# Optimization experiments

Measured on AMD Instinct MI355X. Metric: run time of the kernel, lower is better.

The kernel has to match this reference:

```python
import jax, jax.numpy as jnp
import numpy as np

HIDDEN = 128
OUT_EMB = 256
OUT_CH = 1
NUM_LAYERS = 3
NUM_EDGES = 1000000
NUM_NODES = 50000


def glorot_orthogonal(key, shape, scale=2.0):
    # orthogonal init then rescale variance like DIG's glorot_orthogonal
    W = jax.nn.initializers.orthogonal()(key, shape, jnp.float32)
    W = W * jnp.sqrt(scale / ((shape[0] + shape[1]) * jnp.var(W)))
    return W


def setup_inputs() -> dict:
    key = jax.random.key(0)
    ks = jax.random.split(key, 8)
    e2 = jax.random.normal(ks[0], (NUM_EDGES, HIDDEN), dtype=jnp.float32)
    i = jax.random.randint(ks[1], (NUM_EDGES,), 0, NUM_NODES, dtype=jnp.int64)
    W_up = glorot_orthogonal(ks[2], (OUT_EMB, HIDDEN))
    b_up = jnp.zeros((OUT_EMB,), jnp.float32)
    Ws = jnp.stack([glorot_orthogonal(k, (OUT_EMB, OUT_EMB)) for k in jax.random.split(ks[3], NUM_LAYERS)])
    bs = jnp.zeros((NUM_LAYERS, OUT_EMB), jnp.float32)
    W_out = glorot_orthogonal(ks[4], (OUT_CH, OUT_EMB))
    return {"e2": e2, "i": i, "W_up": W_up, "b_up": b_up,
            "Ws": Ws, "bs": bs, "W_out": W_out, "num_nodes": NUM_NODES}


def reference(e2, i, W_up, b_up, Ws, bs, W_out, num_nodes):
    # scatter-sum edge messages into nodes: v[n] = sum_{k: i[k]==n} e2[k]
    v = jax.ops.segment_sum(e2, i, num_segments=num_nodes)  # [N, HIDDEN]
    v = v @ W_up.T + b_up                                   # [N, OUT_EMB]
    for l in range(NUM_LAYERS):
        v = jax.nn.silu(v @ Ws[l].T + bs[l])
    return v @ W_out.T                                      # [N, OUT_CH]
```

## Files before the change

kernel.cpp:

```cpp
#include <hip/hip_runtime.h>

#define HIDDEN 128
#define OUT_EMB 256
#define NLAYERS 3
#define TM 64
#define LDA 264

typedef __bf16 bf16x8 __attribute__((ext_vector_type(8)));
typedef float f32x4 __attribute__((ext_vector_type(4)));

__device__ __forceinline__ unsigned short f2bf(float x) {
    union { float f; unsigned u; } c; c.f = x;
    unsigned r = c.u + 0x7fff + ((c.u >> 16) & 1);
    return (unsigned short)(r >> 16);
}
__device__ __forceinline__ float bf2f(unsigned short h) {
    union { unsigned u; float f; } c; c.u = ((unsigned)h) << 16;
    return c.f;
}

__global__ __launch_bounds__(256) void hist_kernel(
    const int* __restrict__ idx, int* __restrict__ counts, int ne)
{
    int e = blockIdx.x * 256 + threadIdx.x;
    if (e < ne) atomicAdd(&counts[idx[e]], 1);
}

__global__ __launch_bounds__(256) void scan1_kernel(
    const int* __restrict__ counts, int* __restrict__ bsum, int n)
{
    __shared__ int sh[256];
    int t = threadIdx.x;
    int i = blockIdx.x * 256 + t;
    sh[t] = (i < n) ? counts[i] : 0;
    __syncthreads();
    for (int off = 128; off > 0; off >>= 1) {
        if (t < off) sh[t] += sh[t + off];
        __syncthreads();
    }
    if (t == 0) bsum[blockIdx.x] = sh[0];
}

__global__ __launch_bounds__(256) void scan2_kernel(
    int* __restrict__ bsum, int* __restrict__ boff, int nb)
{
    __shared__ int sh[256];
    int t = threadIdx.x;
    int v = (t < nb) ? bsum[t] : 0;
    sh[t] = v;
    __syncthreads();
    for (int off = 1; off < 256; off <<= 1) {
        int u = (t >= off) ? sh[t - off] : 0;
        __syncthreads();
        sh[t] += u;
        __syncthreads();
    }
    if (t < nb) boff[t] = sh[t] - v;
}

__global__ __launch_bounds__(256) void scan3_kernel(
    const int* __restrict__ counts, const int* __restrict__ boff,
    int* __restrict__ offsets, int* __restrict__ cursor, int n)
{
    __shared__ int sh[256];
    int t = threadIdx.x;
    int i = blockIdx.x * 256 + t;
    int v = (i < n) ? counts[i] : 0;
    sh[t] = v;
    __syncthreads();
    for (int off = 1; off < 256; off <<= 1) {
        int u = (t >= off) ? sh[t - off] : 0;
        __syncthreads();
        sh[t] += u;
        __syncthreads();
    }
    if (i < n) {
        int excl = boff[blockIdx.x] + sh[t] - v;
        offsets[i] = excl;
        cursor[i]  = excl;
    }
}

__global__ __launch_bounds__(256) void fill_kernel(
    const int* __restrict__ idx, int* __restrict__ cursor,
    int* __restrict__ edge_list, int ne)
{
    int e = blockIdx.x * 256 + threadIdx.x;
    if (e < ne) {
        int pos = atomicAdd(&cursor[idx[e]], 1);
        edge_list[pos] = e;
    }
}

__global__ __launch_bounds__(256) void gather_kernel(
    const float* __restrict__ e2, const int* __restrict__ edge_list,
    const int* __restrict__ offsets, const int* __restrict__ counts,
    unsigned short* __restrict__ vbf, int Mpad)
{
    int node = blockIdx.x * 4 + (threadIdx.x >> 6);
    if (node >= Mpad) return;
    int lane = threadIdx.x & 63;
    int half = lane >> 5;
    int c4   = lane & 31;
    int start = offsets[node];
    int cnt   = counts[node];

    f32x4 a0 = {0.f, 0.f, 0.f, 0.f};
    f32x4 a1 = {0.f, 0.f, 0.f, 0.f};

    int j = 0;
    for (; j + 4 <= cnt; j += 4) {
        int e0 = edge_list[start + j + half];
        int e1 = edge_list[start + j + 2 + half];
        f32x4 x0 = *(const f32x4*)(e2 + (long long)e0 * HIDDEN + c4 * 4);
        f32x4 x1 = *(const f32x4*)(e2 + (long long)e1 * HIDDEN + c4 * 4);
        a0 += x0;
        a1 += x1;
    }
    for (; j + 2 <= cnt; j += 2) {
        int e0 = edge_list[start + j + half];
        f32x4 x0 = *(const f32x4*)(e2 + (long long)e0 * HIDDEN + c4 * 4);
        a0 += x0;
    }
    if (j < cnt && half == 0) {
        int e0 = edge_list[start + j];
        f32x4 x0 = *(const f32x4*)(e2 + (long long)e0 * HIDDEN + c4 * 4);
        a1 += x0;
    }
    a0 += a1;
    a0[0] += __shfl_xor(a0[0], 32);
    a0[1] += __shfl_xor(a0[1], 32);
    a0[2] += __shfl_xor(a0[2], 32);
    a0[3] += __shfl_xor(a0[3], 32);

    if (half == 0) {
        unsigned lo = (unsigned)f2bf(a0[0]) | ((unsigned)f2bf(a0[1]) << 16);
        unsigned hi = (unsigned)f2bf(a0[2]) | ((unsigned)f2bf(a0[3]) << 16);
        uint2 p; p.x = lo; p.y = hi;
        *(uint2*)(vbf + (long long)node * HIDDEN + c4 * 4) = p;
    }
}

__global__ __launch_bounds__(256) void convert_kernel(
    const float* __restrict__ wup_f, const float* __restrict__ ws_f,
    unsigned short* __restrict__ wup, unsigned short* __restrict__ wsl)
{
    int t = blockIdx.x * blockDim.x + threadIdx.x;
    const int n1 = OUT_EMB * HIDDEN;
    const int n2 = NLAYERS * OUT_EMB * OUT_EMB;
    if (t < n1) wup[t] = f2bf(wup_f[t]);
    else if (t < n1 + n2) wsl[t - n1] = f2bf(ws_f[t - n1]);
}

__global__ __launch_bounds__(256) void mlp_kernel(
    const unsigned short* __restrict__ vbf,
    const unsigned short* __restrict__ wup,
    const float* __restrict__ bup,
    const unsigned short* __restrict__ wsl,
    const float* __restrict__ bs,
    const float* __restrict__ wout,
    float* __restrict__ out, int M)
{
    __shared__ unsigned short act[TM * LDA];

    const int tid  = threadIdx.x;
    const int wv   = tid >> 6;
    const int lane = tid & 63;
    const int ln15 = lane & 15;
    const int kq   = lane >> 4;
    const int n0   = wv * 64;
    const long long rowbase = (long long)blockIdx.x * TM;

    f32x4 acc[4][4];

    #pragma unroll
    for (int mt = 0; mt < 4; ++mt)
        #pragma unroll
        for (int nt = 0; nt < 4; ++nt)
            acc[mt][nt] = (f32x4){0.f, 0.f, 0.f, 0.f};

    #pragma unroll
    for (int ks = 0; ks < 4; ++ks) {
        bf16x8 a[4], b[4];
        #pragma unroll
        for (int mt = 0; mt < 4; ++mt)
            a[mt] = *(const bf16x8*)&vbf[(rowbase + mt * 16 + ln15) * HIDDEN + ks * 32 + kq * 8];
        #pragma unroll
        for (int nt = 0; nt < 4; ++nt)
            b[nt] = *(const bf16x8*)&wup[(n0 + nt * 16 + ln15) * HIDDEN + ks * 32 + kq * 8];
        #pragma unroll
        for (int mt = 0; mt < 4; ++mt)
            #pragma unroll
            for (int nt = 0; nt < 4; ++nt)
                acc[mt][nt] = __builtin_amdgcn_mfma_f32_16x16x32_bf16(a[mt], b[nt], acc[mt][nt], 0, 0, 0);
    }
    #pragma unroll
    for (int nt = 0; nt < 4; ++nt) {
        int n = n0 + nt * 16 + ln15;
        float bias = bup[n];
        #pragma unroll
        for (int mt = 0; mt < 4; ++mt)
            #pragma unroll
            for (int r = 0; r < 4; ++r)
                act[(mt * 16 + kq * 4 + r) * LDA + n] = f2bf(acc[mt][nt][r] + bias);
    }
    __syncthreads();

    for (int l = 0; l < NLAYERS; ++l) {
        const unsigned short* W = wsl + l * OUT_EMB * OUT_EMB;
        const float* bias_l = bs + l * OUT_EMB;

        #pragma unroll
        for (int mt = 0; mt < 4; ++mt)
            #pragma unroll
            for (int nt = 0; nt < 4; ++nt)
                acc[mt][nt] = (f32x4){0.f, 0.f, 0.f, 0.f};

        #pragma unroll
        for (int ks = 0; ks < 8; ++ks) {
            bf16x8 a[4], b[4];
            #pragma unroll
            for (int mt = 0; mt < 4; ++mt)
                a[mt] = *(const bf16x8*)&act[(mt * 16 + ln15) * LDA + ks * 32 + kq * 8];
            #pragma unroll
            for (int nt = 0; nt < 4; ++nt)
                b[nt] = *(const bf16x8*)&W[(n0 + nt * 16 + ln15) * OUT_EMB + ks * 32 + kq * 8];
            #pragma unroll
            for (int mt = 0; mt < 4; ++mt)
                #pragma unroll
                for (int nt = 0; nt < 4; ++nt)
                    acc[mt][nt] = __builtin_amdgcn_mfma_f32_16x16x32_bf16(a[mt], b[nt], acc[mt][nt], 0, 0, 0);
        }
        __syncthreads();
        #pragma unroll
        for (int nt = 0; nt < 4; ++nt) {
            int n = n0 + nt * 16 + ln15;
            float bias = bias_l[n];
            #pragma unroll
            for (int mt = 0; mt < 4; ++mt)
                #pragma unroll
                for (int r = 0; r < 4; ++r) {
                    float x = acc[mt][nt][r] + bias;
                    float s = x / (1.f + __expf(-x));
                    act[(mt * 16 + kq * 4 + r) * LDA + n] = f2bf(s);
                }
        }
        __syncthreads();
    }

    {
        int r = tid >> 2;
        int part = tid & 3;
        const unsigned short* arow = &act[r * LDA + part * 64];
        const float* wrow = wout + part * 64;
        float s = 0.f;
        #pragma unroll
        for (int jj = 0; jj < 64; ++jj) s += bf2f(arow[jj]) * wrow[jj];
        s += __shfl_xor(s, 1);
        s += __shfl_xor(s, 2);
        long long rowg = rowbase + r;
        if (part == 0 && rowg < M) out[rowg] = s;
    }
}

extern "C" void kernel_launch(void* const* d_in, const int* in_sizes, int n_in,
                              void* d_out, int out_size, void* d_ws, size_t ws_size,
                              hipStream_t stream) {
    const float* e2    = (const float*)d_in[0];
    const int*   idx   = (const int*)d_in[1];
    const float* W_up  = (const float*)d_in[2];
    const float* b_up  = (const float*)d_in[3];
    const float* Ws    = (const float*)d_in[4];
    const float* bs    = (const float*)d_in[5];
    const float* W_out = (const float*)d_in[6];

    const int ne = in_sizes[0] / HIDDEN;
    const int M  = out_size;
    const int Mpad = ((M + TM - 1) / TM) * TM;
    const int nb = (Mpad + 255) / 256;

    char* p = (char*)d_ws;
    unsigned short* vbf    = (unsigned short*)p;  p += (size_t)Mpad * HIDDEN * 2;
    unsigned short* wup_bf = (unsigned short*)p;  p += (size_t)OUT_EMB * HIDDEN * 2;
    unsigned short* wsl_bf = (unsigned short*)p;  p += (size_t)NLAYERS * OUT_EMB * OUT_EMB * 2;
    int* counts    = (int*)p;  p += (size_t)Mpad * 4;
    int* offsets   = (int*)p;  p += (size_t)Mpad * 4;
    int* cursor    = (int*)p;  p += (size_t)Mpad * 4;
    int* bsum      = (int*)p;  p += 256 * 4;
    int* boff      = (int*)p;  p += 256 * 4;
    int* edge_list = (int*)p;  p += (size_t)ne * 4;

    hipMemsetAsync(counts, 0, (size_t)Mpad * 4, stream);

    hist_kernel <<<(ne + 255) / 256, 256, 0, stream>>>(idx, counts, ne);
    scan1_kernel<<<nb, 256, 0, stream>>>(counts, bsum, Mpad);
    scan2_kernel<<<1, 256, 0, stream>>>(bsum, boff, nb);
    scan3_kernel<<<nb, 256, 0, stream>>>(counts, boff, offsets, cursor, Mpad);
    fill_kernel <<<(ne + 255) / 256, 256, 0, stream>>>(idx, cursor, edge_list, ne);

    {
        int total = OUT_EMB * HIDDEN + NLAYERS * OUT_EMB * OUT_EMB;
        convert_kernel<<<(total + 255) / 256, 256, 0, stream>>>(W_up, Ws, wup_bf, wsl_bf);
    }

    gather_kernel<<<(Mpad + 3) / 4, 256, 0, stream>>>(e2, edge_list, offsets, counts, vbf, Mpad);

    mlp_kernel<<<Mpad / TM, 256, 0, stream>>>(vbf, wup_bf, b_up, wsl_bf, bs, W_out,
                                              (float*)d_out, M);
}
```

Measured before the change: 890.5 us.

## Split fused MLP kernel into per-layer GEMM kernels with global activation buffers

Replaces the single fused MLP kernel, which kept activations in shared memory across layers, with separate templated GEMM launches per layer plus a final output-projection kernel. Intermediate activations now round-trip through two global bf16 ping-pong buffers. The likely intent is to cut shared-memory use and register pressure per block to raise occupancy, at the cost of extra global memory traffic and more kernel launches.

```diff
diff --git a/kernel.cpp b/kernel.cpp
--- a/kernel.cpp
+++ b/kernel.cpp
@@ -4,7 +4,6 @@
 #define OUT_EMB 256
 #define NLAYERS 3
 #define TM 64
-#define LDA 264
 
 typedef __bf16 bf16x8 __attribute__((ext_vector_type(8)));
 typedef float f32x4 __attribute__((ext_vector_type(4)));
@@ -152,17 +151,14 @@
     else if (t < n1 + n2) wsl[t - n1] = f2bf(ws_f[t - n1]);
 }
 
-__global__ __launch_bounds__(256) void mlp_kernel(
-    const unsigned short* __restrict__ vbf,
-    const unsigned short* __restrict__ wup,
-    const float* __restrict__ bup,
-    const unsigned short* __restrict__ wsl,
-    const float* __restrict__ bs,
-    const float* __restrict__ wout,
-    float* __restrict__ out, int M)
-{
-    __shared__ unsigned short act[TM * LDA];
-
+template<int K, bool SILU>
+__global__ __launch_bounds__(256) void gemm_kernel(
+    const unsigned short* __restrict__ A,
+    const unsigned short* __restrict__ W,
+    const float* __restrict__ bias,
+    unsigned short* __restrict__ C,
+    int Mpad)
+{
     const int tid  = threadIdx.x;
     const int wv   = tid >> 6;
     const int lane = tid & 63;
@@ -172,95 +168,63 @@
     const long long rowbase = (long long)blockIdx.x * TM;
 
     f32x4 acc[4][4];
-
     #pragma unroll
     for (int mt = 0; mt < 4; ++mt)
         #pragma unroll
         for (int nt = 0; nt < 4; ++nt)
             acc[mt][nt] = (f32x4){0.f, 0.f, 0.f, 0.f};
 
-    #pragma unroll
-    for (int ks = 0; ks < 4; ++ks) {
+    const unsigned short* Abase = A + rowbase * K + ln15 * K + kq * 8;
+    const unsigned short* Wbase = W + (n0 + ln15) * K + kq * 8;
+
+    #pragma unroll
+    for (int ks = 0; ks < K / 32; ++ks) {
         bf16x8 a[4], b[4];
         #pragma unroll
         for (int mt = 0; mt < 4; ++mt)
-            a[mt] = *(const bf16x8*)&vbf[(rowbase + mt * 16 + ln15) * HIDDEN + ks * 32 + kq * 8];
+            a[mt] = *(const bf16x8*)(Abase + (mt * 16) * K + ks * 32);
         #pragma unroll
         for (int nt = 0; nt < 4; ++nt)
-            b[nt] = *(const bf16x8*)&wup[(n0 + nt * 16 + ln15) * HIDDEN + ks * 32 + kq * 8];
+            b[nt] = *(const bf16x8*)(Wbase + (nt * 16) * K + ks * 32);
         #pragma unroll
         for (int mt = 0; mt < 4; ++mt)
             #pragma unroll
             for (int nt = 0; nt < 4; ++nt)
                 acc[mt][nt] = __builtin_amdgcn_mfma_f32_16x16x32_bf16(a[mt], b[nt], acc[mt][nt], 0, 0, 0);
     }
+
     #pragma unroll
     for (int nt = 0; nt < 4; ++nt) {
         int n = n0 + nt * 16 + ln15;
-        float bias = bup[n];
+        float bi = bias[n];
         #pragma unroll
         for (int mt = 0; mt < 4; ++mt)
             #pragma unroll
-            for (int r = 0; r < 4; ++r)
-                act[(mt * 16 + kq * 4 + r) * LDA + n] = f2bf(acc[mt][nt][r] + bias);
-    }
-    __syncthreads();
-
-    for (int l = 0; l < NLAYERS; ++l) {
-        const unsigned short* W = wsl + l * OUT_EMB * OUT_EMB;
-        const float* bias_l = bs + l * OUT_EMB;
-
-        #pragma unroll
-        for (int mt = 0; mt < 4; ++mt)
-            #pragma unroll
-            for (int nt = 0; nt < 4; ++nt)
-                acc[mt][nt] = (f32x4){0.f, 0.f, 0.f, 0.f};
-
-        #pragma unroll
-        for (int ks = 0; ks < 8; ++ks) {
-            bf16x8 a[4], b[4];
-            #pragma unroll
-            for (int mt = 0; mt < 4; ++mt)
-                a[mt] = *(const bf16x8*)&act[(mt * 16 + ln15) * LDA + ks * 32 + kq * 8];
-            #pragma unroll
-            for (int nt = 0; nt < 4; ++nt)
-                b[nt] = *(const bf16x8*)&W[(n0 + nt * 16 + ln15) * OUT_EMB + ks * 32 + kq * 8];
-            #pragma unroll
-            for (int mt = 0; mt < 4; ++mt)
-                #pragma unroll
-                for (int nt = 0; nt < 4; ++nt)
-                    acc[mt][nt] = __builtin_amdgcn_mfma_f32_16x16x32_bf16(a[mt], b[nt], acc[mt][nt], 0, 0, 0);
-        }
-        __syncthreads();
-        #pragma unroll
-        for (int nt = 0; nt < 4; ++nt) {
-            int n = n0 + nt * 16 + ln15;
-            float bias = bias_l[n];
-            #pragma unroll
-            for (int mt = 0; mt < 4; ++mt)
-                #pragma unroll
-                for (int r = 0; r < 4; ++r) {
-                    float x = acc[mt][nt][r] + bias;
-                    float s = x / (1.f + __expf(-x));
-                    act[(mt * 16 + kq * 4 + r) * LDA + n] = f2bf(s);
-                }
-        }
-        __syncthreads();
-    }
-
-    {
-        int r = tid >> 2;
-        int part = tid & 3;
-        const unsigned short* arow = &act[r * LDA + part * 64];
-        const float* wrow = wout + part * 64;
-        float s = 0.f;
-        #pragma unroll
-        for (int jj = 0; jj < 64; ++jj) s += bf2f(arow[jj]) * wrow[jj];
-        s += __shfl_xor(s, 1);
-        s += __shfl_xor(s, 2);
-        long long rowg = rowbase + r;
-        if (part == 0 && rowg < M) out[rowg] = s;
-    }
+            for (int r = 0; r < 4; ++r) {
+                float x = acc[mt][nt][r] + bi;
+                if (SILU) x = x / (1.f + __expf(-x));
+                long long row = rowbase + mt * 16 + kq * 4 + r;
+                C[row * OUT_EMB + n] = f2bf(x);
+            }
+    }
+}
+
+__global__ __launch_bounds__(256) void out_kernel(
+    const unsigned short* __restrict__ A, const float* __restrict__ wout,
+    float* __restrict__ out, int M)
+{
+    int t = blockIdx.x * 256 + threadIdx.x;
+    int r = t >> 2;
+    int part = t & 3;
+    if (r >= M) return;
+    const unsigned short* arow = A + (long long)r * OUT_EMB + part * 64;
+    const float* wrow = wout + part * 64;
+    float s = 0.f;
+    #pragma unroll
+    for (int j = 0; j < 64; ++j) s += bf2f(arow[j]) * wrow[j];
+    s += __shfl_xor(s, 1);
+    s += __shfl_xor(s, 2);
+    if (part == 0) out[r] = s;
 }
 
 extern "C" void kernel_launch(void* const* d_in, const int* in_sizes, int n_in,
@@ -283,6 +247,8 @@
     unsigned short* vbf    = (unsigned short*)p;  p += (size_t)Mpad * HIDDEN * 2;
     unsigned short* wup_bf = (unsigned short*)p;  p += (size_t)OUT_EMB * HIDDEN * 2;
     unsigned short* wsl_bf = (unsigned short*)p;  p += (size_t)NLAYERS * OUT_EMB * OUT_EMB * 2;
+    unsigned short* actA   = (unsigned short*)p;  p += (size_t)Mpad * OUT_EMB * 2;
+    unsigned short* actB   = (unsigned short*)p;  p += (size_t)Mpad * OUT_EMB * 2;
     int* counts    = (int*)p;  p += (size_t)Mpad * 4;
     int* offsets   = (int*)p;  p += (size_t)Mpad * 4;
     int* cursor    = (int*)p;  p += (size_t)Mpad * 4;
@@ -305,6 +271,11 @@
 
     gather_kernel<<<(Mpad + 3) / 4, 256, 0, stream>>>(e2, edge_list, offsets, counts, vbf, Mpad);
 
-    mlp_kernel<<<Mpad / TM, 256, 0, stream>>>(vbf, wup_bf, b_up, wsl_bf, bs, W_out,
-                                              (float*)d_out, M);
-}
+    const int gblocks = Mpad / TM;
+    gemm_kernel<HIDDEN, false><<<gblocks, 256, 0, stream>>>(vbf,  wup_bf,              b_up,  actA, Mpad);
+    gemm_kernel<OUT_EMB, true><<<gblocks, 256, 0, stream>>>(actA, wsl_bf + 0 * OUT_EMB * OUT_EMB, bs + 0 * OUT_EMB, actB, Mpad);
+    gemm_kernel<OUT_EMB, true><<<gblocks, 256, 0, stream>>>(actB, wsl_bf + 1 * OUT_EMB * OUT_EMB, bs + 1 * OUT_EMB, actA, Mpad);
+    gemm_kernel<OUT_EMB, true><<<gblocks, 256, 0, stream>>>(actA, wsl_bf + 2 * OUT_EMB * OUT_EMB, bs + 2 * OUT_EMB, actB, Mpad);
+
+    out_kernel<<<(M * 4 + 255) / 256, 256, 0, stream>>>(actB, W_out, (float*)d_out, M);
+}
```

After: 958.5 us. 7.6% more time.
